# Optimization experiments

Hardware: AMD Instinct MI355X
Metric: run time of the kernel (lower is better)

The kernel has to match this reference:

```python
import jax, jax.numpy as jnp
import numpy as np

B, T, S, D, H, F = 4, 1024, 1024, 1024, 16, 4096
NEG = jnp.float32(-1e9)


def _ln(x, g, b):
    m = jnp.mean(x, axis=-1, keepdims=True)
    v = jnp.mean((x - m) ** 2, axis=-1, keepdims=True)
    return (x - m) * jax.lax.rsqrt(v + 1e-5) * g + b


def _mha(q, k, v, wq, bq, wk, bk, wv, bv, wo, bo, scale, mask, causal, sbias):
    Bq, Tq, Dq = q.shape
    Sk = k.shape[1]
    dk = Dq // H
    Q = (q @ wq.T + bq).reshape(Bq, Tq, H, dk).transpose(0, 2, 1, 3)  # [B,H,T,dk]
    K = (k @ wk.T + bk).reshape(Bq, Sk, H, dk).transpose(0, 2, 1, 3)  # [B,H,S,dk]
    V = (v @ wv.T + bv).reshape(Bq, Sk, H, dk).transpose(0, 2, 1, 3)
    s = jnp.einsum('bhtd,bhsd->bhts', Q, K) / jnp.sqrt(jnp.float32(dk))
    if sbias is not None:
        s = s + scale * sbias[:, None, None, :]
    if mask is not None:
        s = jnp.where(mask == 0, NEG, s)
    if causal is not None:
        s = jnp.where(causal == 0, NEG, s)
    a = jax.nn.softmax(s, axis=-1)
    o = jnp.einsum('bhts,bhsd->bhtd', a, V).transpose(0, 2, 1, 3).reshape(Bq, Tq, Dq)
    return o @ wo.T + bo


def setup_inputs():
    key = jax.random.key(0)
    ks = jax.random.split(key, 16)
    r = lambda i, shape, s=0.02: jax.random.normal(ks[i], shape, dtype=jnp.float32) * s
    z = lambda *shape: jnp.zeros(shape, jnp.float32)
    o = lambda *shape: jnp.ones(shape, jnp.float32)
    inp = dict(
        x=r(0, (B, T, D), 1.0),
        memory=r(1, (B, S, D), 1.0),
        sentence_bias=r(2, (B, S), 1.0),
        trg_mask=jnp.ones((B, 1, 1, T), jnp.int32),
        trg_causal_mask=jnp.tril(jnp.ones((T, T), jnp.int32))[None, None],
        src_mask=jnp.ones((B, 1, 1, S), jnp.int32),
        sa_wq=r(3, (D, D)), sa_bq=z(D), sa_wk=r(4, (D, D)), sa_bk=z(D),
        sa_wv=r(5, (D, D)), sa_bv=z(D), sa_wo=r(6, (D, D)), sa_bo=z(D),
        sa_scale=jnp.float32(0.1),
        ca_wq=r(7, (D, D)), ca_bq=z(D), ca_wk=r(8, (D, D)), ca_bk=z(D),
        ca_wv=r(9, (D, D)), ca_bv=z(D), ca_wo=r(10, (D, D)), ca_bo=z(D),
        ca_scale=jnp.float32(0.1),
        ln1_g=o(D), ln1_b=z(D), ln2_g=o(D), ln2_b=z(D), ln3_g=o(D), ln3_b=z(D),
        ffn_w1=r(11, (F, D)), ffn_b1=z(F), ffn_w2=r(12, (D, F)), ffn_b2=z(D),
    )
    return inp


def reference(x, memory, trg_mask, trg_causal_mask, src_mask, sentence_bias,
              sa_wq, sa_bq, sa_wk, sa_bk, sa_wv, sa_bv, sa_wo, sa_bo, sa_scale,
              ca_wq, ca_bq, ca_wk, ca_bk, ca_wv, ca_bv, ca_wo, ca_bo, ca_scale,
              ln1_g, ln1_b, ln2_g, ln2_b, ln3_g, ln3_b,
              ffn_w1, ffn_b1, ffn_w2, ffn_b2):
    # Faithful quirk: Q comes from normed x, K/V from raw residual stream.
    x = x + _mha(_ln(x, ln1_g, ln1_b), x, x,
                 sa_wq, sa_bq, sa_wk, sa_bk, sa_wv, sa_bv, sa_wo, sa_bo,
                 sa_scale, trg_mask, trg_causal_mask, None)
    x = x + _mha(_ln(x, ln2_g, ln2_b), memory, memory,
                 ca_wq, ca_bq, ca_wk, ca_bk, ca_wv, ca_bv, ca_wo, ca_bo,
                 ca_scale, src_mask, None, sentence_bias)
    h = _ln(x, ln3_g, ln3_b)
    x = x + (jax.nn.relu(h @ ffn_w1.T + ffn_b1) @ ffn_w2.T + ffn_b2)
    return x
```

## Files before the change

### kernel.cpp

```cpp
#include <hip/hip_runtime.h>
#include <hip/hip_bf16.h>
#include <cmath>
#include <stdint.h>

typedef __hip_bfloat16 bf16;
typedef __attribute__((ext_vector_type(8))) __bf16 bf16x8;
typedef __attribute__((ext_vector_type(8))) unsigned short u16x8;
typedef __attribute__((ext_vector_type(4))) float f32x4;

__device__ __forceinline__ void gld16(const void* g, const void* l)
{
    __builtin_amdgcn_global_load_lds(
        (const __attribute__((address_space(1))) unsigned int*)(unsigned long long)g,
        (__attribute__((address_space(3))) unsigned int*)(unsigned int)(unsigned long long)l,
        16, 0, 0);
}

struct CvtSrcs { const float* p[24]; };

__global__ __launch_bounds__(256) void cvt_all(CvtSrcs s, bf16* __restrict__ dst)
{
    const int i = (blockIdx.x * 256 + threadIdx.x) * 8;
    const int seg = i >> 20;
    const float* sp = s.p[seg] + (i & 1048575);
    const float4 a = *(const float4*)(sp);
    const float4 b = *(const float4*)(sp + 4);
    const float v[8] = {a.x, a.y, a.z, a.w, b.x, b.y, b.z, b.w};
    bf16 tmp[8];
#pragma unroll
    for (int j = 0; j < 8; ++j) tmp[j] = __float2bfloat16(v[j]);
    *(uint4*)(dst + i) = *(const uint4*)tmp;
}

enum {
    EPI_QSCALE = 0,
    EPI_KV = 1,
    EPI_RELU = 2,
    EPI_RES_F32_F32OUT = 3,
    EPI_PART = 4
};

template <int EPI>
__global__ __launch_bounds__(512, 2) void gemm256(
    const bf16* __restrict__ A, const bf16* __restrict__ W,
    const float* __restrict__ bias, void* __restrict__ out,
    int N, int Kiter, int Kstride)
{
    __shared__ __align__(16) unsigned short sA[2][2][128 * 64];
    __shared__ __align__(16) unsigned short sB[2][2][128 * 64];

    const int t  = threadIdx.x;
    const int l  = t & 63;
    const int w  = t >> 6;
    const int wv = w * 64;
    const int wr = w >> 2;
    const int wc = w & 3;
    const int lm = l & 15;
    const int kq = l >> 4;
    const int rx = lm & 7;

    int bx = blockIdx.x;
    if (EPI == EPI_PART) {
        const int chunk = bx >> 6;
        bx &= 63;
        A += (size_t)chunk * 1024;
        W += (size_t)chunk * 1024;
        out = (void*)((bf16*)out + (size_t)chunk * 4096 * 1024);
    }
    const int xcd = bx & 7;
    const int ib  = bx >> 3;
    const int bm  = xcd * 2 + (ib & 1);
    const int bn  = ib >> 1;

    const bf16* gA = A + (size_t)(bm * 256 + (t >> 3)) * Kstride
                       + ((t & 7) ^ ((t >> 3) & 7)) * 8;
    const bf16* gB = W + (size_t)(bn * 256 + (t >> 3)) * Kstride
                       + ((t & 7) ^ ((t >> 3) & 7)) * 8;

#define SQA(slot, kt, j)                                        \
    gld16(gA + (size_t)((j) * 64) * Kstride + (kt) * 64,        \
          &sA[slot][(j) >> 1][(((j) & 1) * 512 + wv) * 8])
#define SQB(slot, kt, j)                                        \
    gld16(gB + (size_t)((j) * 64) * Kstride + (kt) * 64,        \
          &sB[slot][(j) >> 1][(((j) & 1) * 512 + wv) * 8])

    bf16x8 af[4][2], bg[2][2];

#define READ_AF(s_, mh)                                                     \
    do {                                                                    \
        _Pragma("unroll")                                                   \
        for (int mi = 0; mi < 4; ++mi)                                      \
            _Pragma("unroll")                                               \
            for (int kk = 0; kk < 2; ++kk) {                                \
                const int lr = (mh) * 64 + mi * 16 + lm;                    \
                const int sl = ((kk << 2) | kq) ^ rx;                       \
                af[mi][kk] = __builtin_bit_cast(bf16x8,                     \
                    *(const u16x8*)(&sA[s_][wr][lr * 64 + sl * 8]));        \
            }                                                               \
    } while (0)
#define READ_BG(s_, nh)                                                     \
    do {                                                                    \
        _Pragma("unroll")                                                   \
        for (int ni = 0; ni < 2; ++ni)                                      \
            _Pragma("unroll")                                               \
            for (int kk = 0; kk < 2; ++kk) {                                \
                const int lr = (wc & 1) * 64 + (nh) * 32 + ni * 16 + lm;    \
                const int sl = ((kk << 2) | kq) ^ rx;                       \
                bg[ni][kk] = __builtin_bit_cast(bf16x8,                     \
                    *(const u16x8*)(&sB[s_][wc >> 1][lr * 64 + sl * 8]));   \
            }                                                               \
    } while (0)
#define MFMA_QUAD(mh, nh)                                                   \
    do {                                                                    \
        __builtin_amdgcn_s_setprio(1);                                      \
        _Pragma("unroll")                                                   \
        for (int mi = 0; mi < 4; ++mi)                                      \
            _Pragma("unroll")                                               \
            for (int ni = 0; ni < 2; ++ni)                                  \
                _Pragma("unroll")                                           \
                for (int kk = 0; kk < 2; ++kk)                              \
                    acc[(mh) * 4 + mi][(nh) * 2 + ni] =                     \
                        __builtin_amdgcn_mfma_f32_16x16x32_bf16(            \
                            af[mi][kk], bg[ni][kk],                         \
                            acc[(mh) * 4 + mi][(nh) * 2 + ni], 0, 0, 0);    \
        __builtin_amdgcn_s_setprio(0);                                      \
    } while (0)
#define BARRIER() do { __builtin_amdgcn_s_barrier();                        \
                       __builtin_amdgcn_sched_barrier(0); } while (0)
#define WAITV2() asm volatile("s_waitcnt vmcnt(2)" ::: "memory")
#define WAITV0() asm volatile("s_waitcnt vmcnt(0)" ::: "memory")

    f32x4 acc[8][4] = {};
    const int NT = Kiter >> 6;

    SQB(0, 0, 0); SQB(0, 0, 1); SQB(0, 0, 2); SQB(0, 0, 3);
    SQA(0, 0, 0); SQA(0, 0, 2); SQA(0, 0, 1); SQA(0, 0, 3);

    for (int tt = 0; tt < NT - 1; ++tt) {
        const int s = tt & 1, d = s ^ 1, kn = tt + 1;
        WAITV2(); BARRIER();
        SQB(d, kn, 0); SQB(d, kn, 1);
        READ_AF(s, 0); READ_BG(s, 0);
        MFMA_QUAD(0, 0);
        WAITV2(); BARRIER();
        SQB(d, kn, 2); SQB(d, kn, 3);
        READ_AF(s, 1);
        MFMA_QUAD(1, 0);
        SQA(d, kn, 0); SQA(d, kn, 2);
        READ_BG(s, 1);
        MFMA_QUAD(1, 1);
        SQA(d, kn, 1); SQA(d, kn, 3);
        READ_AF(s, 0);
        MFMA_QUAD(0, 1);
    }
    {
        const int s = (NT - 1) & 1;
        WAITV2(); BARRIER();
        READ_AF(s, 0); READ_BG(s, 0);
        MFMA_QUAD(0, 0);
        WAITV0(); BARRIER();
        READ_AF(s, 1);
        MFMA_QUAD(1, 0);
        READ_BG(s, 1);
        MFMA_QUAD(1, 1);
        READ_AF(s, 0);
        MFMA_QUAD(0, 1);
    }
#undef SQA
#undef SQB
#undef READ_AF
#undef READ_BG
#undef MFMA_QUAD
#undef BARRIER
#undef WAITV2
#undef WAITV0

    __syncthreads();
    unsigned short* scr = (w < 4) ? &sA[0][0][0] + w * 8192
                                  : &sB[0][0][0] + (w - 4) * 8192;

#pragma unroll
    for (int NI = 0; NI < 4; ++NI) {
        const int col = bn * 256 + wc * 64 + NI * 16 + lm;
        const float bv = (EPI == EPI_PART) ? 0.f : bias[col];
        const int c  = NI * 2 + (lm >> 3);
        const int ci = lm & 7;
#pragma unroll
        for (int MI = 0; MI < 8; ++MI) {
#pragma unroll
            for (int r = 0; r < 4; ++r) {
                float v = acc[MI][NI][r] + bv;
                if (EPI == EPI_RELU) v = fmaxf(v, 0.f);
                const int row = MI * 16 + kq * 4 + r;
                scr[row * 64 + ((c ^ (row & 7)) * 8) + ci] =
                    __builtin_bit_cast(unsigned short, (__bf16)v);
            }
        }
    }
#pragma unroll
    for (int it = 0; it < 16; ++it) {
        const int row = it * 8 + (l >> 3);
        const int lc  = l & 7;
        const u16x8 vv = *(const u16x8*)&scr[row * 64 + ((lc ^ (row & 7)) * 8)];
        const int Crow = bm * 256 + wr * 128 + row;
        const int Ccol = bn * 256 + wc * 64 + lc * 8;
        *(u16x8*)((bf16*)out + (size_t)Crow * N + Ccol) = vv;
    }
}

template <int EPI, int BM>
__global__ __launch_bounds__(BM * 2, 2) void gemm_bt(
    const bf16* __restrict__ A, const bf16* __restrict__ W,
    const float* __restrict__ bias, const float* __restrict__ bias2,
    const float* __restrict__ res, void* __restrict__ out,
    int M, int N, int Kiter, int Kstride)
{
    constexpr int T    = BM * 2;
    constexpr int ISSA = (BM * 4) / T;
    constexpr int ISSB = 512 / T;
    constexpr int ROWS = T / 4;
    constexpr int MBK  = 4096 / BM;
    constexpr int MBX  = MBK / 8;
    constexpr int MBS  = (BM == 64) ? 3 : 2;

    __shared__ __align__(16) unsigned short sA[2][BM * 32];
    __shared__ __align__(16) unsigned short sB[2][128 * 32];

    const int t  = threadIdx.x;
    const int l  = t & 63;
    const int w  = t >> 6;
    const int wv = w * 64;
    const int wm = (w >> 1) * 64;
    const int wn = (w & 1) * 64;
    const int lm = l & 15;
    const int kq = l >> 4;

    int bx = blockIdx.x;
    const int xcd = bx & 7;
    const int ib  = bx >> 3;
    const int bm  = xcd * MBX + (ib & (MBX - 1));
    const int bn  = ib >> MBS;

    const bf16* gA = A + (size_t)(bm * BM + (t >> 2)) * Kstride + (t & 3) * 8;
    const bf16* gB = W + (size_t)(bn * 128 + (t >> 2)) * Kstride + (t & 3) * 8;

    int aoffs[4], boffs[4];
#pragma unroll
    for (int i = 0; i < 4; ++i) {
        aoffs[i] = (wm + i * 16 + lm) * 32 + kq * 8;
        boffs[i] = (wn + i * 16 + lm) * 32 + kq * 8;
    }

#define STAGE(buf, kk)                                                       \
    do {                                                                     \
        _Pragma("unroll")                                                    \
        for (int j = 0; j < ISSA; ++j)                                       \
            gld16(gA + (size_t)j * ROWS * Kstride + (kk),                    \
                  &sA[buf][(j * T + wv) * 8]);                               \
        _Pragma("unroll")                                                    \
        for (int j = 0; j < ISSB; ++j)                                       \
            gld16(gB + (size_t)j * ROWS * Kstride + (kk),                    \
                  &sB[buf][(j * T + wv) * 8]);                               \
    } while (0)

    STAGE(0, 0);
    __syncthreads();

    f32x4 acc[4][4] = {};

    for (int k0 = 0; k0 < Kiter; k0 += 32) {
        const int cur = (k0 >> 5) & 1;

        if (k0 + 32 < Kiter) STAGE(cur ^ 1, k0 + 32);

        bf16x8 af[4], bg[4];
#pragma unroll
        for (int i = 0; i < 4; ++i)
            af[i] = __builtin_bit_cast(bf16x8, *(const u16x8*)(&sA[cur][aoffs[i]]));
#pragma unroll
        for (int i = 0; i < 4; ++i)
            bg[i] = __builtin_bit_cast(bf16x8, *(const u16x8*)(&sB[cur][boffs[i]]));
#pragma unroll
        for (int mi = 0; mi < 4; ++mi)
#pragma unroll
            for (int ni = 0; ni < 4; ++ni)
                acc[mi][ni] = __builtin_amdgcn_mfma_f32_16x16x32_bf16(
                    af[mi], bg[ni], acc[mi][ni], 0, 0, 0);

        __syncthreads();
    }
#undef STAGE

#pragma unroll
    for (int ni = 0; ni < 4; ++ni) {
        const int col = bn * 128 + wn + ni * 16 + lm;
        float bv = 0.f;
        if (EPI == EPI_KV) bv = (col < 1024) ? bias[col] : bias2[col - 1024];
        else bv = bias[col];
#pragma unroll
        for (int mi = 0; mi < 4; ++mi) {
#pragma unroll
            for (int r = 0; r < 4; ++r) {
                const int row = bm * BM + wm + mi * 16 + kq * 4 + r;
                float v = acc[mi][ni][r] + bv;
                if (EPI == EPI_QSCALE) v *= 0.125f;
                if (EPI == EPI_KV) {
                    if (col < 1024) {
                        ((bf16*)out)[(size_t)row * 1024 + col] = __float2bfloat16(v);
                    } else {
                        const int ch = col - 1024;
                        const size_t idx = (size_t)4 * 1048576 +
                            ((size_t)((row >> 10) * 16 + (ch >> 6)) * 64 + (ch & 63)) * 1024
                            + (row & 1023);
                        ((bf16*)out)[idx] = __float2bfloat16(v);
                    }
                } else if (EPI == EPI_RES_F32_F32OUT) {
                    const size_t idx = (size_t)row * N + col;
                    ((float*)out)[idx] = v + res[idx];
                } else {
                    ((bf16*)out)[(size_t)row * N + col] = __float2bfloat16(v);
                }
            }
        }
    }
}

__global__ __launch_bounds__(256) void ffn2_reduce(
    const bf16* __restrict__ P, const float* __restrict__ x2,
    const float* __restrict__ b2, float* __restrict__ out)
{
    const int i = (blockIdx.x * 256 + threadIdx.x) * 8;
    float v[8];
    {
        const float4 a = *(const float4*)(x2 + i);
        const float4 b = *(const float4*)(x2 + i + 4);
        v[0]=a.x; v[1]=a.y; v[2]=a.z; v[3]=a.w; v[4]=b.x; v[5]=b.y; v[6]=b.z; v[7]=b.w;
    }
    const int cb = i & 1023;
#pragma unroll
    for (int j = 0; j < 8; ++j) v[j] += b2[cb + j];
#pragma unroll
    for (int c = 0; c < 4; ++c) {
        const u16x8 u = *(const u16x8*)(P + (size_t)c * 4194304 + i);
        const bf16x8 pb = __builtin_bit_cast(bf16x8, u);
#pragma unroll
        for (int j = 0; j < 8; ++j) v[j] += (float)pb[j];
    }
    float4 o0 = {v[0], v[1], v[2], v[3]}, o1 = {v[4], v[5], v[6], v[7]};
    *(float4*)(out + i) = o0;
    *(float4*)(out + i + 4) = o1;
}

template <bool CAUSAL, bool SBIAS>
__global__ __launch_bounds__(256, 2) void flash_attn(
    const bf16* __restrict__ Q, const bf16* __restrict__ K,
    const bf16* __restrict__ Vt, bf16* __restrict__ O,
    const float* __restrict__ sbias, const float* __restrict__ scale_ptr)
{
    __shared__ __align__(16) unsigned short sK[2][64 * 64];
    __shared__ __align__(16) unsigned short sV[2][64 * 64];
    __shared__ __align__(16) unsigned short sP[4 * 32 * 72];

    const int t  = threadIdx.x;
    const int l  = t & 63;
    const int w  = t >> 6;
    const int wv = w * 64;
    const int lm = l & 15;
    const int kq = l >> 4;

    const int bh = blockIdx.x & 63;
    const int qb = blockIdx.x >> 6;
    const int h  = bh & 15;
    const int b  = bh >> 4;

    const int tb = qb * 128 + w * 32;
    const size_t qrow0 = (size_t)(b * 1024 + tb) * 1024 + h * 64;

    bf16x8 qf[2][2];
#pragma unroll
    for (int mi = 0; mi < 2; ++mi)
#pragma unroll
        for (int kk = 0; kk < 2; ++kk)
            qf[mi][kk] = __builtin_bit_cast(bf16x8,
                *(const u16x8*)(Q + qrow0 + (size_t)(mi * 16 + lm) * 1024 + kk * 32 + kq * 8));

    float cs = 0.f; const float* sb = nullptr;
    if (SBIAS) { cs = scale_ptr[0]; sb = sbias + b * 1024; }

    const bf16* gK = K  + (size_t)(b * 1024 + (t >> 3)) * 1024 + h * 64
                   + ((t & 7) ^ ((t >> 3) & 7)) * 8;
    const bf16* gV = Vt + (size_t)((b * 16 + h) * 64 + (t >> 3)) * 1024
                   + ((t & 7) ^ ((t >> 3) & 7)) * 8;
    __bf16* sPw = (__bf16*)sP + w * 32 * 72;

#define STAGE_KV(buf, s0r)                                                   \
    do {                                                                     \
        gld16(gK + (size_t)(s0r) * 1024,        &sK[buf][wv * 8]);           \
        gld16(gK + (size_t)((s0r) + 32) * 1024, &sK[buf][2048 + wv * 8]);    \
        gld16(gV + (s0r),                       &sV[buf][wv * 8]);           \
        gld16(gV + (s0r) + 32 * 1024,           &sV[buf][2048 + wv * 8]);    \
    } while (0)

    const int niter = CAUSAL ? (2 * qb + 2) : 16;

    STAGE_KV(0, 0);
    __syncthreads();

    f32x4 acc_o[2][4] = {};
    f32x4 l_run[2] = {};

    for (int it = 0; it < niter; ++it) {
        const int s0 = it * 64;
        const int cur = it & 1;

        if (it + 1 < niter) STAGE_KV(cur ^ 1, s0 + 64);

        f32x4 accs[2][4] = {};
#pragma unroll
        for (int ni = 0; ni < 4; ++ni)
#pragma unroll
            for (int kk = 0; kk < 2; ++kk) {
                const bf16x8 kf = __builtin_bit_cast(bf16x8,
                    *(const u16x8*)(&sK[cur][(ni * 16 + lm) * 64
                        + ((((kk << 2) | kq)) ^ (lm & 7)) * 8]));
#pragma unroll
                for (int mi = 0; mi < 2; ++mi)
                    accs[mi][ni] = __builtin_amdgcn_mfma_f32_16x16x32_bf16(
                        qf[mi][kk], kf, accs[mi][ni], 0, 0, 0);
            }

        if (SBIAS) {
#pragma unroll
            for (int ni = 0; ni < 4; ++ni) {
                const float sv = cs * sb[s0 + ni * 16 + lm];
#pragma unroll
                for (int mi = 0; mi < 2; ++mi)
#pragma unroll
                    for (int r = 0; r < 4; ++r) accs[mi][ni][r] += sv;
            }
        }
        if (CAUSAL && (s0 + 63 > tb)) {
#pragma unroll
            for (int ni = 0; ni < 4; ++ni) {
                const int s = s0 + ni * 16 + lm;
#pragma unroll
                for (int mi = 0; mi < 2; ++mi)
#pragma unroll
                    for (int r = 0; r < 4; ++r)
                        if (s > tb + mi * 16 + kq * 4 + r) accs[mi][ni][r] = -1e30f;
            }
        }

#pragma unroll
        for (int mi = 0; mi < 2; ++mi)
#pragma unroll
            for (int ni = 0; ni < 4; ++ni)
#pragma unroll
                for (int r = 0; r < 4; ++r) {
                    const float e = __expf(accs[mi][ni][r]);
                    l_run[mi][r] += e;
                    sPw[(mi * 16 + kq * 4 + r) * 72 + ni * 16 + lm] = (__bf16)e;
                }

#pragma unroll
        for (int kk = 0; kk < 2; ++kk) {
            bf16x8 pf[2];
#pragma unroll
            for (int mi = 0; mi < 2; ++mi)
                pf[mi] = __builtin_bit_cast(bf16x8,
                    *(const u16x8*)(sPw + (mi * 16 + lm) * 72 + kk * 32 + kq * 8));
#pragma unroll
            for (int di = 0; di < 4; ++di) {
                const bf16x8 vf = __builtin_bit_cast(bf16x8,
                    *(const u16x8*)(&sV[cur][(di * 16 + lm) * 64
                        + ((((kk << 2) | kq)) ^ (lm & 7)) * 8]));
#pragma unroll
                for (int mi = 0; mi < 2; ++mi)
                    acc_o[mi][di] = __builtin_amdgcn_mfma_f32_16x16x32_bf16(
                        pf[mi], vf, acc_o[mi][di], 0, 0, 0);
            }
        }

        __syncthreads();
    }
#undef STAGE_KV

#pragma unroll
    for (int mi = 0; mi < 2; ++mi) {
        f32x4 lt = l_run[mi];
#pragma unroll
        for (int x = 1; x < 16; x <<= 1)
#pragma unroll
            for (int r = 0; r < 4; ++r) lt[r] += __shfl_xor(lt[r], x, 64);
#pragma unroll
        for (int r = 0; r < 4; ++r) lt[r] = 1.f / lt[r];
#pragma unroll
        for (int di = 0; di < 4; ++di)
#pragma unroll
            for (int r = 0; r < 4; ++r) {
                const size_t idx = (size_t)(b * 1024 + tb + mi * 16 + kq * 4 + r) * 1024
                                 + h * 64 + di * 16 + lm;
                O[idx] = __float2bfloat16(acc_o[mi][di][r] * lt[r]);
            }
    }
}

__global__ __launch_bounds__(256) void ln_kernel(
    const float* __restrict__ xin, const float* __restrict__ g,
    const float* __restrict__ bta, bf16* __restrict__ out)
{
    const int row = blockIdx.x;
    const int t = threadIdx.x;
    const size_t base = (size_t)row * 1024 + t * 4;

    const float4 f = *(const float4*)(xin + base);
    const float v[4] = {f.x, f.y, f.z, f.w};
    float s1 = v[0] + v[1] + v[2] + v[3];
    float s2 = v[0]*v[0] + v[1]*v[1] + v[2]*v[2] + v[3]*v[3];
#pragma unroll
    for (int off = 32; off > 0; off >>= 1) {
        s1 += __shfl_xor(s1, off, 64);
        s2 += __shfl_xor(s2, off, 64);
    }
    __shared__ float r1[4], r2[4];
    if ((t & 63) == 0) { r1[t >> 6] = s1; r2[t >> 6] = s2; }
    __syncthreads();
    s1 = r1[0] + r1[1] + r1[2] + r1[3];
    s2 = r2[0] + r2[1] + r2[2] + r2[3];
    const float mean = s1 * (1.f / 1024.f);
    const float var  = s2 * (1.f / 1024.f) - mean * mean;
    const float rstd = rsqrtf(var + 1e-5f);
#pragma unroll
    for (int j = 0; j < 4; ++j) {
        const int c = t * 4 + j;
        out[base + j] = __float2bfloat16((v[j] - mean) * rstd * g[c] + bta[c]);
    }
}

extern "C" void kernel_launch(void* const* d_in, const int* in_sizes, int n_in,
                              void* d_out, int out_size, void* d_ws, size_t ws_size,
                              hipStream_t stream)
{
    const float* x       = (const float*)d_in[0];
    const float* memory  = (const float*)d_in[1];
    const float* sbias   = (const float*)d_in[2];
    const float* sa_bq = (const float*)d_in[7];
    const float* sa_bk = (const float*)d_in[9];
    const float* sa_bv = (const float*)d_in[11];
    const float* sa_bo = (const float*)d_in[13];
    const float* ca_bq = (const float*)d_in[16];
    const float* ca_bk = (const float*)d_in[18];
    const float* ca_bv = (const float*)d_in[20];
    const float* ca_bo = (const float*)d_in[22];
    const float* ca_scale = (const float*)d_in[23];
    const float* ln1_g = (const float*)d_in[24]; const float* ln1_b = (const float*)d_in[25];
    const float* ln2_g = (const float*)d_in[26]; const float* ln2_b = (const float*)d_in[27];
    const float* ln3_g = (const float*)d_in[28]; const float* ln3_b = (const float*)d_in[29];
    const float* b1 = (const float*)d_in[31];
    const float* b2 = (const float*)d_in[33];

    char* ws = (char*)d_ws;
    const size_t MB = (size_t)1 << 20;
    float* x1    = (float*)(ws + 0 * MB);
    float* x2    = (float*)(ws + 16 * MB);
    bf16* lnbuf  = (bf16*)(ws + 32 * MB);
    bf16* Qb     = (bf16*)(ws + 40 * MB);
    bf16* Kb     = (bf16*)(ws + 48 * MB);
    bf16* Vtb    = (bf16*)(ws + 56 * MB);
    bf16* Ob     = (bf16*)(ws + 64 * MB);
    bf16* ffnmid = (bf16*)(ws + 40 * MB);
    bf16* wx     = (bf16*)(ws + 72 * MB);
    bf16* wmem   = (bf16*)(ws + 80 * MB);
    bf16* bw     = (bf16*)(ws + 88 * MB);
    bf16* b_sa_wq = bw + 0 * 1048576, *b_sa_wk = bw + 1 * 1048576;
    bf16* b_sa_wo = bw + 3 * 1048576;
    bf16* b_ca_wq = bw + 4 * 1048576, *b_ca_wk = bw + 5 * 1048576;
    bf16* b_ca_wo = bw + 7 * 1048576;
    bf16* b_w1   = (bf16*)(ws + 104 * MB);
    bf16* b_w2   = (bf16*)(ws + 112 * MB);
    bf16* part   = (bf16*)(ws + 72 * MB);

    const int M = 4096;
    dim3 blk256(256), blk128(128), blk512(512);
    const dim3 gQ(512);
    const dim3 gKV(512);
    const dim3 gFA(512);
    const dim3 g256(256);

    CvtSrcs cs;
    for (int c = 0; c < 4; ++c) {
        cs.p[c]      = x + (size_t)c * 1048576;
        cs.p[4 + c]  = memory + (size_t)c * 1048576;
        cs.p[16 + c] = (const float*)d_in[30] + (size_t)c * 1048576;
        cs.p[20 + c] = (const float*)d_in[32] + (size_t)c * 1048576;
    }
    cs.p[8]  = (const float*)d_in[6];
    cs.p[9]  = (const float*)d_in[8];
    cs.p[10] = (const float*)d_in[10];
    cs.p[11] = (const float*)d_in[12];
    cs.p[12] = (const float*)d_in[15];
    cs.p[13] = (const float*)d_in[17];
    cs.p[14] = (const float*)d_in[19];
    cs.p[15] = (const float*)d_in[21];
    cvt_all<<<24 * 1048576 / 2048, blk256, 0, stream>>>(cs, wx);

    ln_kernel<<<4096, blk256, 0, stream>>>(x, ln1_g, ln1_b, lnbuf);
    gemm_bt<EPI_QSCALE, 64><<<gQ, blk128, 0, stream>>>(
        lnbuf, b_sa_wq, sa_bq, nullptr, nullptr, Qb, M, 1024, 1024, 1024);
    gemm_bt<EPI_KV, 128><<<gKV, blk256, 0, stream>>>(
        wx, b_sa_wk, sa_bk, sa_bv, nullptr, Kb, M, 2048, 1024, 1024);
    flash_attn<true, false><<<gFA, blk256, 0, stream>>>(Qb, Kb, Vtb, Ob, nullptr, nullptr);
    gemm_bt<EPI_RES_F32_F32OUT, 64><<<gQ, blk128, 0, stream>>>(
        Ob, b_sa_wo, sa_bo, nullptr, x, x1, M, 1024, 1024, 1024);

    ln_kernel<<<4096, blk256, 0, stream>>>(x1, ln2_g, ln2_b, lnbuf);
    gemm_bt<EPI_QSCALE, 64><<<gQ, blk128, 0, stream>>>(
        lnbuf, b_ca_wq, ca_bq, nullptr, nullptr, Qb, M, 1024, 1024, 1024);
    gemm_bt<EPI_KV, 128><<<gKV, blk256, 0, stream>>>(
        wmem, b_ca_wk, ca_bk, ca_bv, nullptr, Kb, M, 2048, 1024, 1024);
    flash_attn<false, true><<<gFA, blk256, 0, stream>>>(Qb, Kb, Vtb, Ob, sbias, ca_scale);
    gemm_bt<EPI_RES_F32_F32OUT, 64><<<gQ, blk128, 0, stream>>>(
        Ob, b_ca_wo, ca_bo, nullptr, x1, x2, M, 1024, 1024, 1024);

    ln_kernel<<<4096, blk256, 0, stream>>>(x2, ln3_g, ln3_b, lnbuf);
    gemm256<EPI_RELU><<<g256, blk512, 0, stream>>>(
        lnbuf, b_w1, b1, ffnmid, 4096, 1024, 1024);
    gemm256<EPI_PART><<<g256, blk512, 0, stream>>>(
        ffnmid, b_w2, nullptr, part, 1024, 1024, 4096);
    ffn2_reduce<<<2048, blk256, 0, stream>>>(part, x2, b2, (float*)d_out);
}
```

Before: 483.0 us.

## Rewrite gemm_bt as 128x128 BK64 pipelined kernel with swizzled LDS

Replaces the simple double-buffered BK=32 gemm_bt (BM 64 or 128) with a fixed 128x128 tile, BK=64 kernel. It interleaves global-to-LDS loads with MFMA quarter-blocks using fine-grained vmcnt waits and barriers, the same way gemm256 does, and XOR-swizzles the LDS layout to avoid bank conflicts. The Q and O-projection GEMMs now launch 256 blocks of 256 threads instead of 512 blocks of 128. The aim is better latency hiding and fewer barriers per K step, at the cost of more LDS per block and fewer blocks for the smaller GEMMs.

```diff
diff --git a/kernel.cpp b/kernel.cpp
--- a/kernel.cpp
+++ b/kernel.cpp
@@ -127,6 +127,7 @@
     } while (0)
 #define BARRIER() do { __builtin_amdgcn_s_barrier();                        \
                        __builtin_amdgcn_sched_barrier(0); } while (0)
+#define WAITV4() asm volatile("s_waitcnt vmcnt(4)" ::: "memory")
 #define WAITV2() asm volatile("s_waitcnt vmcnt(2)" ::: "memory")
 #define WAITV0() asm volatile("s_waitcnt vmcnt(0)" ::: "memory")
 
@@ -166,14 +167,6 @@
         READ_AF(s, 0);
         MFMA_QUAD(0, 1);
     }
-#undef SQA
-#undef SQB
-#undef READ_AF
-#undef READ_BG
-#undef MFMA_QUAD
-#undef BARRIER
-#undef WAITV2
-#undef WAITV0
 
     __syncthreads();
     unsigned short* scr = (w < 4) ? &sA[0][0][0] + w * 8192
@@ -206,25 +199,22 @@
         const int Ccol = bn * 256 + wc * 64 + lc * 8;
         *(u16x8*)((bf16*)out + (size_t)Crow * N + Ccol) = vv;
     }
-}
-
-template <int EPI, int BM>
-__global__ __launch_bounds__(BM * 2, 2) void gemm_bt(
+#undef SQA
+#undef SQB
+#undef READ_AF
+#undef READ_BG
+#undef MFMA_QUAD
+}
+
+template <int EPI>
+__global__ __launch_bounds__(256, 2) void gemm_bt(
     const bf16* __restrict__ A, const bf16* __restrict__ W,
     const float* __restrict__ bias, const float* __restrict__ bias2,
     const float* __restrict__ res, void* __restrict__ out,
     int M, int N, int Kiter, int Kstride)
 {
-    constexpr int T    = BM * 2;
-    constexpr int ISSA = (BM * 4) / T;
-    constexpr int ISSB = 512 / T;
-    constexpr int ROWS = T / 4;
-    constexpr int MBK  = 4096 / BM;
-    constexpr int MBX  = MBK / 8;
-    constexpr int MBS  = (BM == 64) ? 3 : 2;
-
-    __shared__ __align__(16) unsigned short sA[2][BM * 32];
-    __shared__ __align__(16) unsigned short sB[2][128 * 32];
+    __shared__ __align__(16) unsigned short sA[2][128 * 64];
+    __shared__ __align__(16) unsigned short sB[2][128 * 64];
 
     const int t  = threadIdx.x;
     const int l  = t & 63;
@@ -234,62 +224,113 @@
     const int wn = (w & 1) * 64;
     const int lm = l & 15;
     const int kq = l >> 4;
-
-    int bx = blockIdx.x;
+    const int rx = lm & 7;
+
+    const int bx  = blockIdx.x;
     const int xcd = bx & 7;
     const int ib  = bx >> 3;
-    const int bm  = xcd * MBX + (ib & (MBX - 1));
-    const int bn  = ib >> MBS;
-
-    const bf16* gA = A + (size_t)(bm * BM + (t >> 2)) * Kstride + (t & 3) * 8;
-    const bf16* gB = W + (size_t)(bn * 128 + (t >> 2)) * Kstride + (t & 3) * 8;
-
-    int aoffs[4], boffs[4];
-#pragma unroll
-    for (int i = 0; i < 4; ++i) {
-        aoffs[i] = (wm + i * 16 + lm) * 32 + kq * 8;
-        boffs[i] = (wn + i * 16 + lm) * 32 + kq * 8;
-    }
-
-#define STAGE(buf, kk)                                                       \
-    do {                                                                     \
-        _Pragma("unroll")                                                    \
-        for (int j = 0; j < ISSA; ++j)                                       \
-            gld16(gA + (size_t)j * ROWS * Kstride + (kk),                    \
-                  &sA[buf][(j * T + wv) * 8]);                               \
-        _Pragma("unroll")                                                    \
-        for (int j = 0; j < ISSB; ++j)                                       \
-            gld16(gB + (size_t)j * ROWS * Kstride + (kk),                    \
-                  &sB[buf][(j * T + wv) * 8]);                               \
+    const int bm  = xcd * 4 + (ib & 3);
+    const int bn  = ib >> 2;
+
+    const bf16* gA = A + (size_t)(bm * 128 + (t >> 3)) * Kstride
+                       + ((t & 7) ^ ((t >> 3) & 7)) * 8;
+    const bf16* gB = W + (size_t)(bn * 128 + (t >> 3)) * Kstride
+                       + ((t & 7) ^ ((t >> 3) & 7)) * 8;
+
+#define SQA(slot, kt, j)                                        \
+    gld16(gA + (size_t)((j) * 32) * Kstride + (kt) * 64,        \
+          &sA[slot][((j) * 256 + wv) * 8])
+#define SQB(slot, kt, j)                                        \
+    gld16(gB + (size_t)((j) * 32) * Kstride + (kt) * 64,        \
+          &sB[slot][((j) * 256 + wv) * 8])
+
+    bf16x8 af[2][2], bg[2][2];
+
+#define READ_AF(s_, mh)                                                     \
+    do {                                                                    \
+        _Pragma("unroll")                                                   \
+        for (int mi = 0; mi < 2; ++mi)                                      \
+            _Pragma("unroll")                                               \
+            for (int kk = 0; kk < 2; ++kk) {                                \
+                const int lr = wm + (mh) * 32 + mi * 16 + lm;               \
+                const int sl = ((kk << 2) | kq) ^ rx;                       \
+                af[mi][kk] = __builtin_bit_cast(bf16x8,                     \
+                    *(const u16x8*)(&sA[s_][lr * 64 + sl * 8]));            \
+            }                                                               \
     } while (0)
-
-    STAGE(0, 0);
-    __syncthreads();
+#define READ_BG(s_, nh)                                                     \
+    do {                                                                    \
+        _Pragma("unroll")                                                   \
+        for (int ni = 0; ni < 2; ++ni)                                      \
+            _Pragma("unroll")                                               \
+            for (int kk = 0; kk < 2; ++kk) {                                \
+                const int lr = wn + (nh) * 32 + ni * 16 + lm;               \
+                const int sl = ((kk << 2) | kq) ^ rx;                       \
+                bg[ni][kk] = __builtin_bit_cast(bf16x8,                     \
+                    *(const u16x8*)(&sB[s_][lr * 64 + sl * 8]));            \
+            }                                                               \
+    } while (0)
+#define MFMA_QUAD(mh, nh)                                                   \
+    do {                                                                    \
+        __builtin_amdgcn_s_setprio(1);                                      \
+        _Pragma("unroll")                                                   \
+        for (int mi = 0; mi < 2; ++mi)                                      \
+            _Pragma("unroll")                                               \
+            for (int ni = 0; ni < 2; ++ni)                                  \
+                _Pragma("unroll")                                           \
+                for (int kk = 0; kk < 2; ++kk)                              \
+                    acc[(mh) * 2 + mi][(nh) * 2 + ni] =                     \
+                        __builtin_amdgcn_mfma_f32_16x16x32_bf16(            \
+                            af[mi][kk], bg[ni][kk],                         \
+                            acc[(mh) * 2 + mi][(nh) * 2 + ni], 0, 0, 0);    \
+        __builtin_amdgcn_s_setprio(0);                                      \
+    } while (0)
 
     f32x4 acc[4][4] = {};
-
-    for (int k0 = 0; k0 < Kiter; k0 += 32) {
-        const int cur = (k0 >> 5) & 1;
-
-        if (k0 + 32 < Kiter) STAGE(cur ^ 1, k0 + 32);
-
-        bf16x8 af[4], bg[4];
-#pragma unroll
-        for (int i = 0; i < 4; ++i)
-            af[i] = __builtin_bit_cast(bf16x8, *(const u16x8*)(&sA[cur][aoffs[i]]));
-#pragma unroll
-        for (int i = 0; i < 4; ++i)
-            bg[i] = __builtin_bit_cast(bf16x8, *(const u16x8*)(&sB[cur][boffs[i]]));
-#pragma unroll
-        for (int mi = 0; mi < 4; ++mi)
-#pragma unroll
-            for (int ni = 0; ni < 4; ++ni)
-                acc[mi][ni] = __builtin_amdgcn_mfma_f32_16x16x32_bf16(
-                    af[mi], bg[ni], acc[mi][ni], 0, 0, 0);
-
-        __syncthreads();
-    }
-#undef STAGE
+    const int NT = Kiter >> 6;
+
+    SQB(0, 0, 0); SQB(0, 0, 2); SQA(0, 0, 0); SQA(0, 0, 2);
+    SQB(0, 0, 1); SQB(0, 0, 3); SQA(0, 0, 1); SQA(0, 0, 3);
+
+    for (int tt = 0; tt < NT - 1; ++tt) {
+        const int s = tt & 1, d = s ^ 1, kn = tt + 1;
+        WAITV4(); BARRIER();
+        SQB(d, kn, 0); SQB(d, kn, 2);
+        READ_AF(s, 0); READ_BG(s, 0);
+        MFMA_QUAD(0, 0);
+        WAITV2(); BARRIER();
+        SQA(d, kn, 0); SQA(d, kn, 2);
+        READ_AF(s, 1);
+        MFMA_QUAD(1, 0);
+        SQB(d, kn, 1); SQB(d, kn, 3);
+        READ_BG(s, 1);
+        MFMA_QUAD(1, 1);
+        SQA(d, kn, 1); SQA(d, kn, 3);
+        READ_AF(s, 0);
+        MFMA_QUAD(0, 1);
+    }
+    {
+        const int s = (NT - 1) & 1;
+        WAITV4(); BARRIER();
+        READ_AF(s, 0); READ_BG(s, 0);
+        MFMA_QUAD(0, 0);
+        WAITV0(); BARRIER();
+        READ_AF(s, 1);
+        MFMA_QUAD(1, 0);
+        READ_BG(s, 1);
+        MFMA_QUAD(1, 1);
+        READ_AF(s, 0);
+        MFMA_QUAD(0, 1);
+    }
+#undef SQA
+#undef SQB
+#undef READ_AF
+#undef READ_BG
+#undef MFMA_QUAD
+#undef BARRIER
+#undef WAITV4
+#undef WAITV2
+#undef WAITV0
 
 #pragma unroll
     for (int ni = 0; ni < 4; ++ni) {
@@ -301,7 +342,7 @@
         for (int mi = 0; mi < 4; ++mi) {
 #pragma unroll
             for (int r = 0; r < 4; ++r) {
-                const int row = bm * BM + wm + mi * 16 + kq * 4 + r;
+                const int row = bm * 128 + wm + mi * 16 + kq * 4 + r;
                 float v = acc[mi][ni][r] + bv;
                 if (EPI == EPI_QSCALE) v *= 0.125f;
                 if (EPI == EPI_KV) {
@@ -581,8 +622,8 @@
     bf16* part   = (bf16*)(ws + 72 * MB);
 
     const int M = 4096;
-    dim3 blk256(256), blk128(128), blk512(512);
-    const dim3 gQ(512);
+    dim3 blk256(256), blk512(512);
+    const dim3 gQ(256);
     const dim3 gKV(512);
     const dim3 gFA(512);
     const dim3 g256(256);
@@ -605,21 +646,21 @@
     cvt_all<<<24 * 1048576 / 2048, blk256, 0, stream>>>(cs, wx);
 
     ln_kernel<<<4096, blk256, 0, stream>>>(x, ln1_g, ln1_b, lnbuf);
-    gemm_bt<EPI_QSCALE, 64><<<gQ, blk128, 0, stream>>>(
+    gemm_bt<EPI_QSCALE><<<gQ, blk256, 0, stream>>>(
         lnbuf, b_sa_wq, sa_bq, nullptr, nullptr, Qb, M, 1024, 1024, 1024);
-    gemm_bt<EPI_KV, 128><<<gKV, blk256, 0, stream>>>(
+    gemm_bt<EPI_KV><<<gKV, blk256, 0, stream>>>(
         wx, b_sa_wk, sa_bk, sa_bv, nullptr, Kb, M, 2048, 1024, 1024);
     flash_attn<true, false><<<gFA, blk256, 0, stream>>>(Qb, Kb, Vtb, Ob, nullptr, nullptr);
-    gemm_bt<EPI_RES_F32_F32OUT, 64><<<gQ, blk128, 0, stream>>>(
+    gemm_bt<EPI_RES_F32_F32OUT><<<gQ, blk256, 0, stream>>>(
         Ob, b_sa_wo, sa_bo, nullptr, x, x1, M, 1024, 1024, 1024);
 
     ln_kernel<<<4096, blk256, 0, stream>>>(x1, ln2_g, ln2_b, lnbuf);
-    gemm_bt<EPI_QSCALE, 64><<<gQ, blk128, 0, stream>>>(
+    gemm_bt<EPI_QSCALE><<<gQ, blk256, 0, stream>>>(
         lnbuf, b_ca_wq, ca_bq, nullptr, nullptr, Qb, M, 1024, 1024, 1024);
-    gemm_bt<EPI_KV, 128><<<gKV, blk256, 0, stream>>>(
+    gemm_bt<EPI_KV><<<gKV, blk256, 0, stream>>>(
         wmem, b_ca_wk, ca_bk, ca_bv, nullptr, Kb, M, 2048, 1024, 1024);
     flash_attn<false, true><<<gFA, blk256, 0, stream>>>(Qb, Kb, Vtb, Ob, sbias, ca_scale);
-    gemm_bt<EPI_RES_F32_F32OUT, 64><<<gQ, blk128, 0, stream>>>(
+    gemm_bt<EPI_RES_F32_F32OUT><<<gQ, blk256, 0, stream>>>(
         Ob, b_ca_wo, ca_bo, nullptr, x1, x2, M, 1024, 1024, 1024);
 
     ln_kernel<<<4096, blk256, 0, stream>>>(x2, ln3_g, ln3_b, lnbuf);
```

Result: no change. 478.1 us (-1.0%).
